# Kernel optimization log

Hardware: AMD Instinct MI355X
Metric: run time of the kernel (lower is better)

## Reference

```python
import jax, jax.numpy as jnp
import numpy as np

B, T, E = 4, 2_000_000, 8
C, K, STRIDE = 128, 512, 512
CHUNK, OVERLAP = 64000, 511  # overlap defaults to kernel_size - 1


def _candidate_positions(T):
    """Exact set of window start positions visited by the chunked streaming max.

    Replays the chunk loop of _lowmem_max_over_time: chunk starts advance by
    step = chunk_size - overlap (not a multiple of stride!), and within each
    chunk conv windows start at chunk_start + stride*k.
    """
    step = max(1, CHUNK - OVERLAP)
    pos = []
    start = 0
    while start < T:
        end = min(start + CHUNK, T)
        end_ext = min(end + OVERLAP, T)
        L = end_ext - start
        if L >= K:
            n = (L - K) // STRIDE + 1
            pos.append(start + STRIDE * np.arange(n, dtype=np.int64))
        if end == T:
            break
        start += step
    p = np.unique(np.concatenate(pos))
    return np.clip(p, 0, max(0, T - K))


POS = _candidate_positions(T)                       # [P] static window starts
WIN_IDX = POS[:, None] + np.arange(K, dtype=np.int64)  # [P, K] gather indices


def setup_inputs() -> dict:
    key = jax.random.key(0)
    ks = jax.random.split(key, 5)
    scale = 1.0 / float(np.sqrt(E * K))  # torch Conv1d default init range
    return {
        "x": jax.random.normal(ks[0], (B, T, E), dtype=jnp.float32),
        "w1": jax.random.uniform(ks[1], (C, E, K), jnp.float32, -scale, scale),
        "b1": jax.random.uniform(ks[2], (C,), jnp.float32, -scale, scale),
        "w2": jax.random.uniform(ks[3], (C, E, K), jnp.float32, -scale, scale),
        "b2": jax.random.uniform(ks[4], (C,), jnp.float32, -scale, scale),
    }


def reference(x, w1, b1, w2, b2):
    # Gather every candidate window the chunked scan would see: [B, P, K, E]
    wins = x[:, WIN_IDX, :]
    # Original clones windows under no_grad (stop_grad_input=True): input gets no grad.
    wins = jax.lax.stop_gradient(wins)
    # Gated conv (GLU): conv1(z) * sigmoid(conv2(z)) at each window -> [B, C, P]
    c1 = jnp.einsum('bpke,cek->bcp', wins, w1) + b1[:, None]
    c2 = jnp.einsum('bpke,cek->bcp', wins, w2) + b2[:, None]
    g = c1 * jax.nn.sigmoid(c2)
    # Global max-over-time per (batch, channel); identical value to the
    # running-max pass followed by exact re-evaluation at argmax positions.
    return g.max(axis=-1)  # [B, C]
```

## Files before the change

### kernel.cpp

```cpp
#include <hip/hip_runtime.h>


#define T_LEN 2000000
#define P_CNT 3937
#define M_TOT 15748
#define KD    4096

typedef __attribute__((ext_vector_type(8))) short short8;
typedef __attribute__((ext_vector_type(4))) float f32x4;

static __device__ __forceinline__ unsigned short f2bf(float f) {
    unsigned u = __builtin_bit_cast(unsigned, f);
    unsigned r = (u + 0x7FFFu + ((u >> 16) & 1u)) >> 16;
    return (unsigned short)r;
}

static __device__ __forceinline__ unsigned ordenc(float f) {
    unsigned u = __builtin_bit_cast(unsigned, f);
    return (u & 0x80000000u) ? ~u : (u | 0x80000000u);
}

static __device__ __forceinline__ size_t row_base(int m) {
    if (m > M_TOT - 1) m = M_TOT - 1;
    int bb = m / P_CNT;
    int p  = m - bb * P_CNT;
    int j, kp;
    if (p < 3875) { j = p / 125; kp = p - j * 125; }
    else          { j = 31;      kp = p - 3875; }
    long pos = (long)j * 63489 + (long)kp * 512;
    return ((size_t)bb * T_LEN + (size_t)pos) * 8u;
}

#define GLD_LDS16(gp, lp)                                                      \
    __builtin_amdgcn_global_load_lds(                                          \
        (const __attribute__((address_space(1))) void*)(gp),                   \
        (__attribute__((address_space(3))) void*)(lp), 16, 0, 0)

__global__ __launch_bounds__(256) void pack_w(const float* __restrict__ w1,
                                              const float* __restrict__ w2,
                                              unsigned short* __restrict__ Bp,
                                              unsigned* __restrict__ outu) {
    int idx = blockIdx.x * 256 + threadIdx.x;
    if (idx < 512) outu[idx] = 0u;
    if (idx >= 256 * KD) return;
    int n = idx >> 12;
    int k = idx & 4095;
    int e = k & 7;
    int t = k >> 3;
    const float* src = (n < 128) ? w1 : w2;
    Bp[idx] = f2bf(src[(n & 127) * 4096 + e * 512 + t]);
}

__global__ __launch_bounds__(512, 4) void gemm_max(const float* __restrict__ x,
                                                   const unsigned short* __restrict__ Bp,
                                                   const float* __restrict__ b1,
                                                   const float* __restrict__ b2,
                                                   unsigned* __restrict__ outu) {
    __shared__ __align__(16) char smem[73728];

    const int t  = threadIdx.x;
    const int m0 = blockIdx.x * 32;

    const int w    = t >> 6;
    const int lane = t & 63;
    const int wm   = w >> 2;
    const int wn   = w & 3;

    const int rA  = t >> 4;
    const int kcA = t & 15;
    const size_t aoff  = row_base(m0 + rA) + (size_t)(kcA * 4);
    const int    awoff = (rA * 128 + kcA * 8) ^ ((rA & 7) << 4);

    const unsigned short* bsrc[4];
    int bdst[4];
#pragma unroll
    for (int i = 0; i < 4; ++i) {
        int d  = i * 8192 + w * 1024 + lane * 16;
        int n  = d >> 7;
        int kc = ((d >> 4) & 7) ^ (n & 7);
        bsrc[i] = Bp + n * KD + kc * 8;
        bdst[i] = i * 8192 + w * 1024;
    }

    f32x4 acc[4];
#pragma unroll
    for (int nf = 0; nf < 4; ++nf) acc[nf] = (f32x4){0.f, 0.f, 0.f, 0.f};

    {
        float4 a0 = *(const float4*)(x + aoff);
#pragma unroll
        for (int i = 0; i < 4; ++i) GLD_LDS16(bsrc[i], smem + 8192 + bdst[i]);
        ushort4 h;
        h.x = f2bf(a0.x); h.y = f2bf(a0.y); h.z = f2bf(a0.z); h.w = f2bf(a0.w);
        *(ushort4*)(smem + awoff) = h;
    }
    __syncthreads();

    for (int ks = 0; ks < 64; ++ks) {
        const int cur = ks & 1;
        const int As  = cur * 4096;
        const int Bs  = 8192 + cur * 32768;
        float4 an;
        if (ks < 63) {
            const int kk = (ks + 1) * 64;
            an = *(const float4*)(x + aoff + kk);
            const int Bsn = 8192 + (cur ^ 1) * 32768;
#pragma unroll
            for (int i = 0; i < 4; ++i) GLD_LDS16(bsrc[i] + kk, smem + Bsn + bdst[i]);
        }
#pragma unroll
        for (int kq = 0; kq < 2; ++kq) {
            short8 af, bfr[4];
            {
                int r    = wm * 16 + (lane & 15);
                int boff = (r * 128 + kq * 64 + (lane >> 4) * 16) ^ ((r & 7) << 4);
                af = *(const short8*)(smem + As + boff);
            }
#pragma unroll
            for (int nf = 0; nf < 4; ++nf) {
                int n    = wn * 64 + nf * 16 + (lane & 15);
                int boff = (n * 128 + kq * 64 + (lane >> 4) * 16) ^ ((n & 7) << 4);
                bfr[nf] = *(const short8*)(smem + Bs + boff);
            }
#pragma unroll
            for (int nf = 0; nf < 4; ++nf)
                acc[nf] = __builtin_amdgcn_mfma_f32_16x16x32_bf16(
                    af, bfr[nf], acc[nf], 0, 0, 0);
        }
        if (ks < 63) {
            const int Asn = (cur ^ 1) * 4096;
            ushort4 h;
            h.x = f2bf(an.x); h.y = f2bf(an.y); h.z = f2bf(an.z); h.w = f2bf(an.w);
            *(ushort4*)(smem + Asn + awoff) = h;
        }
        __syncthreads();
    }

    float* gt = (float*)smem;
#pragma unroll
    for (int nf = 0; nf < 4; ++nf) {
        int col = wn * 64 + nf * 16 + (lane & 15);
#pragma unroll
        for (int q = 0; q < 4; ++q) {
            int row = wm * 16 + (lane >> 4) * 4 + q;
            gt[row * 256 + col] = acc[nf][q];
        }
    }
    __syncthreads();

    if (t < 128) {
        const int   c   = t;
        const float bb1 = b1[c];
        const float bb2 = b2[c];
        int   bprev = (m0 < M_TOT ? m0 : M_TOT - 1) / P_CNT;
        float best  = -3.4e38f;
        for (int r = 0; r < 32; ++r) {
            int m = m0 + r;
            if (m > M_TOT - 1) m = M_TOT - 1;
            int bb = m / P_CNT;
            float c1 = gt[r * 256 + c] + bb1;
            float c2 = gt[r * 256 + 128 + c] + bb2;
            float g  = c1 / (1.f + __expf(-c2));
            if (bb != bprev) {
                atomicMax(&outu[bprev * 128 + c], ordenc(best));
                bprev = bb;
                best  = -3.4e38f;
            }
            best = fmaxf(best, g);
        }
        atomicMax(&outu[bprev * 128 + c], ordenc(best));
    }
}

__global__ __launch_bounds__(256) void unmap_out(unsigned* __restrict__ outu) {
    int i = blockIdx.x * 256 + threadIdx.x;
    if (i < 512) {
        unsigned u = outu[i];
        outu[i] = (u & 0x80000000u) ? (u ^ 0x80000000u) : ~u;
    }
}

extern "C" void kernel_launch(void* const* d_in, const int* in_sizes, int n_in,
                              void* d_out, int out_size, void* d_ws, size_t ws_size,
                              hipStream_t stream) {
    const float* x  = (const float*)d_in[0];
    const float* w1 = (const float*)d_in[1];
    const float* b1 = (const float*)d_in[2];
    const float* w2 = (const float*)d_in[3];
    const float* b2 = (const float*)d_in[4];

    unsigned short* Bp   = (unsigned short*)d_ws;
    unsigned*       outu = (unsigned*)d_out;

    pack_w<<<dim3((256 * KD) / 256), dim3(256), 0, stream>>>(w1, w2, Bp, outu);

    const int nblk = (M_TOT + 31) / 32;
    gemm_max<<<dim3(nblk), dim3(512), 0, stream>>>(x, Bp, b1, b2, outu);

    unmap_out<<<dim3(2), dim3(256), 0, stream>>>(outu);
}
```

Before: 84.61 us.

## Load fp32 A tile directly to LDS via global_load_lds with manual vmcnt waits

```diff
diff --git a/kernel.cpp b/kernel.cpp
--- a/kernel.cpp
+++ b/kernel.cpp
@@ -35,6 +35,12 @@
     __builtin_amdgcn_global_load_lds(                                          \
         (const __attribute__((address_space(1))) void*)(gp),                   \
         (__attribute__((address_space(3))) void*)(lp), 16, 0, 0)
+
+#define FENCE()   asm volatile("" ::: "memory")
+#define WAITVM5() asm volatile("s_waitcnt vmcnt(5)" ::: "memory")
+#define WAITVM0() asm volatile("s_waitcnt vmcnt(0)" ::: "memory")
+#define WAITLGKM0() asm volatile("s_waitcnt lgkmcnt(0)" ::: "memory")
+#define BARRIER() do { FENCE(); __builtin_amdgcn_s_barrier(); FENCE(); } while (0)
 
 __global__ __launch_bounds__(256) void pack_w(const float* __restrict__ w1,
                                               const float* __restrict__ w2,
@@ -56,7 +62,7 @@
                                                    const float* __restrict__ b1,
                                                    const float* __restrict__ b2,
                                                    unsigned* __restrict__ outu) {
-    __shared__ __align__(16) char smem[73728];
+    __shared__ __align__(16) char smem[81920];
 
     const int t  = threadIdx.x;
     const int m0 = blockIdx.x * 32;
@@ -66,10 +72,9 @@
     const int wm   = w >> 2;
     const int wn   = w & 3;
 
-    const int rA  = t >> 4;
-    const int kcA = t & 15;
-    const size_t aoff  = row_base(m0 + rA) + (size_t)(kcA * 4);
-    const int    awoff = (rA * 128 + kcA * 8) ^ ((rA & 7) << 4);
+    const int    rowA  = t >> 4;
+    const size_t asrc0 = row_base(m0 + rowA) + (size_t)((((t & 15) ^ (rowA & 7)) * 4));
+    const int    adst  = w * 1024;
 
     const unsigned short* bsrc[4];
     int bdst[4];
@@ -86,55 +91,67 @@
 #pragma unroll
     for (int nf = 0; nf < 4; ++nf) acc[nf] = (f32x4){0.f, 0.f, 0.f, 0.f};
 
-    {
-        float4 a0 = *(const float4*)(x + aoff);
-#pragma unroll
-        for (int i = 0; i < 4; ++i) GLD_LDS16(bsrc[i], smem + 8192 + bdst[i]);
-        ushort4 h;
-        h.x = f2bf(a0.x); h.y = f2bf(a0.y); h.z = f2bf(a0.z); h.w = f2bf(a0.w);
-        *(ushort4*)(smem + awoff) = h;
-    }
-    __syncthreads();
+    const int rA    = wm * 16 + (lane & 15);
+    const int qA    = lane >> 4;
+    int aro[2];
+#pragma unroll
+    for (int kq = 0; kq < 2; ++kq)
+        aro[kq] = (rA * 256 + kq * 128 + qA * 32) ^ ((rA & 7) << 4);
+    int bro[2][4];
+#pragma unroll
+    for (int kq = 0; kq < 2; ++kq)
+#pragma unroll
+        for (int nf = 0; nf < 4; ++nf) {
+            int n = wn * 64 + nf * 16 + (lane & 15);
+            bro[kq][nf] = (n * 128 + kq * 64 + (lane >> 4) * 16) ^ ((n & 7) << 4);
+        }
+
+#pragma unroll
+    for (int i = 0; i < 4; ++i) GLD_LDS16(bsrc[i], smem + 16384 + bdst[i]);
+    GLD_LDS16(x + asrc0, smem + adst);
+    FENCE();
 
     for (int ks = 0; ks < 64; ++ks) {
         const int cur = ks & 1;
-        const int As  = cur * 4096;
-        const int Bs  = 8192 + cur * 32768;
-        float4 an;
+        const int As  = cur * 8192;
+        const int Bs  = 16384 + cur * 32768;
         if (ks < 63) {
-            const int kk = (ks + 1) * 64;
-            an = *(const float4*)(x + aoff + kk);
-            const int Bsn = 8192 + (cur ^ 1) * 32768;
+            const int kk  = (ks + 1) * 64;
+            const int Asn = (cur ^ 1) * 8192;
+            const int Bsn = 16384 + (cur ^ 1) * 32768;
 #pragma unroll
             for (int i = 0; i < 4; ++i) GLD_LDS16(bsrc[i] + kk, smem + Bsn + bdst[i]);
-        }
+            GLD_LDS16(x + asrc0 + kk, smem + Asn + adst);
+            FENCE();
+            WAITVM5();
+        } else {
+            WAITVM0();
+        }
+        BARRIER();
+
 #pragma unroll
         for (int kq = 0; kq < 2; ++kq) {
-            short8 af, bfr[4];
-            {
-                int r    = wm * 16 + (lane & 15);
-                int boff = (r * 128 + kq * 64 + (lane >> 4) * 16) ^ ((r & 7) << 4);
-                af = *(const short8*)(smem + As + boff);
-            }
-#pragma unroll
-            for (int nf = 0; nf < 4; ++nf) {
-                int n    = wn * 64 + nf * 16 + (lane & 15);
-                int boff = (n * 128 + kq * 64 + (lane >> 4) * 16) ^ ((n & 7) << 4);
-                bfr[nf] = *(const short8*)(smem + Bs + boff);
-            }
+            float4 f0 = *(const float4*)(smem + As + aro[kq]);
+            float4 f1 = *(const float4*)(smem + As + (aro[kq] ^ 16));
+            short8 af;
+            af[0] = (short)f2bf(f0.x); af[1] = (short)f2bf(f0.y);
+            af[2] = (short)f2bf(f0.z); af[3] = (short)f2bf(f0.w);
+            af[4] = (short)f2bf(f1.x); af[5] = (short)f2bf(f1.y);
+            af[6] = (short)f2bf(f1.z); af[7] = (short)f2bf(f1.w);
+            short8 bfr[4];
+#pragma unroll
+            for (int nf = 0; nf < 4; ++nf)
+                bfr[nf] = *(const short8*)(smem + Bs + bro[kq][nf]);
 #pragma unroll
             for (int nf = 0; nf < 4; ++nf)
                 acc[nf] = __builtin_amdgcn_mfma_f32_16x16x32_bf16(
                     af, bfr[nf], acc[nf], 0, 0, 0);
         }
-        if (ks < 63) {
-            const int Asn = (cur ^ 1) * 4096;
-            ushort4 h;
-            h.x = f2bf(an.x); h.y = f2bf(an.y); h.z = f2bf(an.z); h.w = f2bf(an.w);
-            *(ushort4*)(smem + Asn + awoff) = h;
-        }
-        __syncthreads();
-    }
+        WAITLGKM0();
+        BARRIER();
+    }
+
+    __syncthreads();
 
     float* gt = (float*)smem;
 #pragma unroll
```

Result: slower. 93.98 us (+11.1%).

## Prefetch A tile two stages ahead with manual waitcnt barriers

Applied to the files above, without the earlier changes.

```diff
diff --git a/kernel.cpp b/kernel.cpp
--- a/kernel.cpp
+++ b/kernel.cpp
@@ -35,6 +35,11 @@
     __builtin_amdgcn_global_load_lds(                                          \
         (const __attribute__((address_space(1))) void*)(gp),                   \
         (__attribute__((address_space(3))) void*)(lp), 16, 0, 0)
+
+#define FENCE()     asm volatile("" ::: "memory")
+#define WAITVM1()   asm volatile("s_waitcnt vmcnt(1)" ::: "memory")
+#define WAITVM0()   asm volatile("s_waitcnt vmcnt(0)" ::: "memory")
+#define WAITLGKM0() asm volatile("s_waitcnt lgkmcnt(0)" ::: "memory")
 
 __global__ __launch_bounds__(256) void pack_w(const float* __restrict__ w1,
                                               const float* __restrict__ w2,
@@ -66,10 +71,10 @@
     const int wm   = w >> 2;
     const int wn   = w & 3;
 
-    const int rA  = t >> 4;
+    const int rAs = t >> 4;
     const int kcA = t & 15;
-    const size_t aoff  = row_base(m0 + rA) + (size_t)(kcA * 4);
-    const int    awoff = (rA * 128 + kcA * 8) ^ ((rA & 7) << 4);
+    const size_t aoff  = row_base(m0 + rAs) + (size_t)(kcA * 4);
+    const int    awoff = (rAs * 128 + kcA * 8) ^ ((rAs & 7) << 4);
 
     const unsigned short* bsrc[4];
     int bdst[4];
@@ -86,54 +91,80 @@
 #pragma unroll
     for (int nf = 0; nf < 4; ++nf) acc[nf] = (f32x4){0.f, 0.f, 0.f, 0.f};
 
+    const int rA = wm * 16 + (lane & 15);
+    int aro[2];
+#pragma unroll
+    for (int kq = 0; kq < 2; ++kq)
+        aro[kq] = (rA * 128 + kq * 64 + (lane >> 4) * 16) ^ ((rA & 7) << 4);
+    int bro[2][4];
+#pragma unroll
+    for (int kq = 0; kq < 2; ++kq)
+#pragma unroll
+        for (int nf = 0; nf < 4; ++nf) {
+            int n = wn * 64 + nf * 16 + (lane & 15);
+            bro[kq][nf] = (n * 128 + kq * 64 + (lane >> 4) * 16) ^ ((n & 7) << 4);
+        }
+
+#pragma unroll
+    for (int i = 0; i < 4; ++i) GLD_LDS16(bsrc[i], smem + 8192 + bdst[i]);
+    FENCE();
+    float4 a0 = *(const float4*)(x + aoff);
+    FENCE();
+    float4 anext = *(const float4*)(x + aoff + 64);
+    FENCE();
     {
-        float4 a0 = *(const float4*)(x + aoff);
-#pragma unroll
-        for (int i = 0; i < 4; ++i) GLD_LDS16(bsrc[i], smem + 8192 + bdst[i]);
         ushort4 h;
         h.x = f2bf(a0.x); h.y = f2bf(a0.y); h.z = f2bf(a0.z); h.w = f2bf(a0.w);
         *(ushort4*)(smem + awoff) = h;
     }
-    __syncthreads();
+    WAITLGKM0();
+    FENCE();
+    __builtin_amdgcn_s_barrier();
+    FENCE();
 
     for (int ks = 0; ks < 64; ++ks) {
         const int cur = ks & 1;
         const int As  = cur * 4096;
         const int Bs  = 8192 + cur * 32768;
-        float4 an;
+        const int Asn = (cur ^ 1) * 4096;
+        const int Bsn = 8192 + (cur ^ 1) * 32768;
+
         if (ks < 63) {
             const int kk = (ks + 1) * 64;
-            an = *(const float4*)(x + aoff + kk);
-            const int Bsn = 8192 + (cur ^ 1) * 32768;
 #pragma unroll
             for (int i = 0; i < 4; ++i) GLD_LDS16(bsrc[i] + kk, smem + Bsn + bdst[i]);
         }
+        FENCE();
+        float4 anext2 = anext;
+        if (ks < 62) anext2 = *(const float4*)(x + aoff + (size_t)(ks + 2) * 64);
+        FENCE();
+
 #pragma unroll
         for (int kq = 0; kq < 2; ++kq) {
-            short8 af, bfr[4];
-            {
-                int r    = wm * 16 + (lane & 15);
-                int boff = (r * 128 + kq * 64 + (lane >> 4) * 16) ^ ((r & 7) << 4);
-                af = *(const short8*)(smem + As + boff);
-            }
-#pragma unroll
-            for (int nf = 0; nf < 4; ++nf) {
-                int n    = wn * 64 + nf * 16 + (lane & 15);
-                int boff = (n * 128 + kq * 64 + (lane >> 4) * 16) ^ ((n & 7) << 4);
-                bfr[nf] = *(const short8*)(smem + Bs + boff);
-            }
+            short8 af = *(const short8*)(smem + As + aro[kq]);
+            short8 bfr[4];
+#pragma unroll
+            for (int nf = 0; nf < 4; ++nf)
+                bfr[nf] = *(const short8*)(smem + Bs + bro[kq][nf]);
 #pragma unroll
             for (int nf = 0; nf < 4; ++nf)
                 acc[nf] = __builtin_amdgcn_mfma_f32_16x16x32_bf16(
                     af, bfr[nf], acc[nf], 0, 0, 0);
         }
+
         if (ks < 63) {
-            const int Asn = (cur ^ 1) * 4096;
             ushort4 h;
-            h.x = f2bf(an.x); h.y = f2bf(an.y); h.z = f2bf(an.z); h.w = f2bf(an.w);
+            h.x = f2bf(anext.x); h.y = f2bf(anext.y);
+            h.z = f2bf(anext.z); h.w = f2bf(anext.w);
             *(ushort4*)(smem + Asn + awoff) = h;
         }
-        __syncthreads();
+        anext = anext2;
+
+        if (ks < 62) { WAITVM1(); } else { WAITVM0(); }
+        WAITLGKM0();
+        FENCE();
+        __builtin_amdgcn_s_barrier();
+        FENCE();
     }
 
     float* gt = (float*)smem;
```

Result: no change. 85.57 us (+1.1%).

## Drop LDS staging; load MFMA fragments directly from global with register double-buffering

Applied to the files above, without the earlier changes.

```diff
diff --git a/kernel.cpp b/kernel.cpp
--- a/kernel.cpp
+++ b/kernel.cpp
@@ -31,121 +31,132 @@
     return ((size_t)bb * T_LEN + (size_t)pos) * 8u;
 }
 
-#define GLD_LDS16(gp, lp)                                                      \
-    __builtin_amdgcn_global_load_lds(                                          \
-        (const __attribute__((address_space(1))) void*)(gp),                   \
-        (__attribute__((address_space(3))) void*)(lp), 16, 0, 0)
+static __device__ __forceinline__ short8 cvt8(float4 lo, float4 hi) {
+    unsigned d0, d1, d2, d3;
+    asm("v_cvt_pk_bf16_f32 %0, %1, %2" : "=v"(d0) : "v"(lo.x), "v"(lo.y));
+    asm("v_cvt_pk_bf16_f32 %0, %1, %2" : "=v"(d1) : "v"(lo.z), "v"(lo.w));
+    asm("v_cvt_pk_bf16_f32 %0, %1, %2" : "=v"(d2) : "v"(hi.x), "v"(hi.y));
+    asm("v_cvt_pk_bf16_f32 %0, %1, %2" : "=v"(d3) : "v"(hi.z), "v"(hi.w));
+    uint4 u; u.x = d0; u.y = d1; u.z = d2; u.w = d3;
+    return __builtin_bit_cast(short8, u);
+}
 
 __global__ __launch_bounds__(256) void pack_w(const float* __restrict__ w1,
                                               const float* __restrict__ w2,
-                                              unsigned short* __restrict__ Bp,
+                                              uint4* __restrict__ Bpf,
                                               unsigned* __restrict__ outu) {
-    int idx = blockIdx.x * 256 + threadIdx.x;
-    if (idx < 512) outu[idx] = 0u;
-    if (idx >= 256 * KD) return;
-    int n = idx >> 12;
-    int k = idx & 4095;
-    int e = k & 7;
-    int t = k >> 3;
+    int c = blockIdx.x * 256 + threadIdx.x;
+    if (c < 512) outu[c] = 0u;
+    if (c >= 131072) return;
+    int l  = c & 63;
+    int nt = (c >> 6) & 15;
+    int kq = (c >> 10) & 1;
+    int ks = c >> 11;
+    int n  = nt * 16 + (l & 15);
+    int kb = ks * 64 + kq * 32 + ((l >> 4) << 3);
     const float* src = (n < 128) ? w1 : w2;
-    Bp[idx] = f2bf(src[(n & 127) * 4096 + e * 512 + t]);
-}
-
-__global__ __launch_bounds__(512, 4) void gemm_max(const float* __restrict__ x,
-                                                   const unsigned short* __restrict__ Bp,
+    int cc = n & 127;
+    unsigned short h[8];
+#pragma unroll
+    for (int j = 0; j < 8; ++j) {
+        int k = kb + j;
+        h[j] = f2bf(src[cc * 4096 + (k & 7) * 512 + (k >> 3)]);
+    }
+    uint4 v;
+    v.x = (unsigned)h[0] | ((unsigned)h[1] << 16);
+    v.y = (unsigned)h[2] | ((unsigned)h[3] << 16);
+    v.z = (unsigned)h[4] | ((unsigned)h[5] << 16);
+    v.w = (unsigned)h[6] | ((unsigned)h[7] << 16);
+    Bpf[c] = v;
+}
+
+#define LOAD_A(FA, ks)                                                         \
+    do {                                                                       \
+        _Pragma("unroll")                                                      \
+        for (int mf = 0; mf < 2; ++mf) {                                       \
+            const char* ab = xb + (mf ? a1 : a0) + (size_t)((ks) * 256);       \
+            _Pragma("unroll")                                                  \
+            for (int kq = 0; kq < 2; ++kq) {                                   \
+                FA[mf][kq][0] = *(const float4*)(ab + kq * 128);               \
+                FA[mf][kq][1] = *(const float4*)(ab + kq * 128 + 16);          \
+            }                                                                  \
+        }                                                                      \
+    } while (0)
+
+#define LOAD_B(BB, ks)                                                         \
+    do {                                                                       \
+        _Pragma("unroll")                                                      \
+        for (int kq = 0; kq < 2; ++kq)                                         \
+            _Pragma("unroll")                                                  \
+            for (int nf = 0; nf < 4; ++nf)                                     \
+                BB[kq][nf] = Bq[((ks) * 2 + kq) * 1024 + bbase + nf * 64];     \
+    } while (0)
+
+#define COMPUTE(FA, BB)                                                        \
+    do {                                                                       \
+        _Pragma("unroll")                                                      \
+        for (int kq = 0; kq < 2; ++kq) {                                       \
+            short8 af0 = cvt8(FA[0][kq][0], FA[0][kq][1]);                     \
+            short8 af1 = cvt8(FA[1][kq][0], FA[1][kq][1]);                     \
+            _Pragma("unroll")                                                  \
+            for (int nf = 0; nf < 4; ++nf) {                                   \
+                short8 bf = __builtin_bit_cast(short8, BB[kq][nf]);            \
+                acc[0][nf] = __builtin_amdgcn_mfma_f32_16x16x32_bf16(          \
+                    af0, bf, acc[0][nf], 0, 0, 0);                             \
+                acc[1][nf] = __builtin_amdgcn_mfma_f32_16x16x32_bf16(          \
+                    af1, bf, acc[1][nf], 0, 0, 0);                             \
+            }                                                                  \
+        }                                                                      \
+    } while (0)
+
+__global__ __launch_bounds__(256, 2) void gemm_max(const float* __restrict__ x,
+                                                   const uint4* __restrict__ Bq,
                                                    const float* __restrict__ b1,
                                                    const float* __restrict__ b2,
                                                    unsigned* __restrict__ outu) {
-    __shared__ __align__(16) char smem[73728];
-
-    const int t  = threadIdx.x;
-    const int m0 = blockIdx.x * 32;
-
-    const int w    = t >> 6;
+    __shared__ float gt[32 * 256];
+
+    const int t    = threadIdx.x;
     const int lane = t & 63;
-    const int wm   = w >> 2;
-    const int wn   = w & 3;
-
-    const int rA  = t >> 4;
-    const int kcA = t & 15;
-    const size_t aoff  = row_base(m0 + rA) + (size_t)(kcA * 4);
-    const int    awoff = (rA * 128 + kcA * 8) ^ ((rA & 7) << 4);
-
-    const unsigned short* bsrc[4];
-    int bdst[4];
-#pragma unroll
-    for (int i = 0; i < 4; ++i) {
-        int d  = i * 8192 + w * 1024 + lane * 16;
-        int n  = d >> 7;
-        int kc = ((d >> 4) & 7) ^ (n & 7);
-        bsrc[i] = Bp + n * KD + kc * 8;
-        bdst[i] = i * 8192 + w * 1024;
-    }
-
-    f32x4 acc[4];
-#pragma unroll
-    for (int nf = 0; nf < 4; ++nf) acc[nf] = (f32x4){0.f, 0.f, 0.f, 0.f};
-
-    {
-        float4 a0 = *(const float4*)(x + aoff);
-#pragma unroll
-        for (int i = 0; i < 4; ++i) GLD_LDS16(bsrc[i], smem + 8192 + bdst[i]);
-        ushort4 h;
-        h.x = f2bf(a0.x); h.y = f2bf(a0.y); h.z = f2bf(a0.z); h.w = f2bf(a0.w);
-        *(ushort4*)(smem + awoff) = h;
-    }
-    __syncthreads();
-
-    for (int ks = 0; ks < 64; ++ks) {
-        const int cur = ks & 1;
-        const int As  = cur * 4096;
-        const int Bs  = 8192 + cur * 32768;
-        float4 an;
-        if (ks < 63) {
-            const int kk = (ks + 1) * 64;
-            an = *(const float4*)(x + aoff + kk);
-            const int Bsn = 8192 + (cur ^ 1) * 32768;
-#pragma unroll
-            for (int i = 0; i < 4; ++i) GLD_LDS16(bsrc[i] + kk, smem + Bsn + bdst[i]);
+    const int wn   = t >> 6;
+    const int m0   = blockIdx.x * 32;
+
+    const char*  xb = (const char*)x;
+    const size_t a0 = row_base(m0 + (lane & 15)) * 4 + (size_t)((lane >> 4) * 32);
+    const size_t a1 = row_base(m0 + 16 + (lane & 15)) * 4 + (size_t)((lane >> 4) * 32);
+    const int bbase = wn * 4 * 64 + lane;
+
+    f32x4 acc[2][4];
+#pragma unroll
+    for (int mf = 0; mf < 2; ++mf)
+#pragma unroll
+        for (int nf = 0; nf < 4; ++nf) acc[mf][nf] = (f32x4){0.f, 0.f, 0.f, 0.f};
+
+    float4 fAX[2][2][2], fAY[2][2][2];
+    uint4  bBX[2][4],    bBY[2][4];
+
+    LOAD_A(fAX, 0);
+    LOAD_B(bBX, 0);
+
+#pragma unroll 2
+    for (int ks = 0; ks < 64; ks += 2) {
+        if (ks + 1 < 64) { LOAD_A(fAY, ks + 1); LOAD_B(bBY, ks + 1); }
+        COMPUTE(fAX, bBX);
+        if (ks + 2 < 64) { LOAD_A(fAX, ks + 2); LOAD_B(bBX, ks + 2); }
+        COMPUTE(fAY, bBY);
+    }
+
+#pragma unroll
+    for (int mf = 0; mf < 2; ++mf)
+#pragma unroll
+        for (int nf = 0; nf < 4; ++nf) {
+            int col = wn * 64 + nf * 16 + (lane & 15);
+#pragma unroll
+            for (int q = 0; q < 4; ++q) {
+                int row = mf * 16 + (lane >> 4) * 4 + q;
+                gt[row * 256 + col] = acc[mf][nf][q];
+            }
         }
-#pragma unroll
-        for (int kq = 0; kq < 2; ++kq) {
-            short8 af, bfr[4];
-            {
-                int r    = wm * 16 + (lane & 15);
-                int boff = (r * 128 + kq * 64 + (lane >> 4) * 16) ^ ((r & 7) << 4);
-                af = *(const short8*)(smem + As + boff);
-            }
-#pragma unroll
-            for (int nf = 0; nf < 4; ++nf) {
-                int n    = wn * 64 + nf * 16 + (lane & 15);
-                int boff = (n * 128 + kq * 64 + (lane >> 4) * 16) ^ ((n & 7) << 4);
-                bfr[nf] = *(const short8*)(smem + Bs + boff);
-            }
-#pragma unroll
-            for (int nf = 0; nf < 4; ++nf)
-                acc[nf] = __builtin_amdgcn_mfma_f32_16x16x32_bf16(
-                    af, bfr[nf], acc[nf], 0, 0, 0);
-        }
-        if (ks < 63) {
-            const int Asn = (cur ^ 1) * 4096;
-            ushort4 h;
-            h.x = f2bf(an.x); h.y = f2bf(an.y); h.z = f2bf(an.z); h.w = f2bf(an.w);
-            *(ushort4*)(smem + Asn + awoff) = h;
-        }
-        __syncthreads();
-    }
-
-    float* gt = (float*)smem;
-#pragma unroll
-    for (int nf = 0; nf < 4; ++nf) {
-        int col = wn * 64 + nf * 16 + (lane & 15);
-#pragma unroll
-        for (int q = 0; q < 4; ++q) {
-            int row = wm * 16 + (lane >> 4) * 4 + q;
-            gt[row * 256 + col] = acc[nf][q];
-        }
-    }
     __syncthreads();
 
     if (t < 128) {
@@ -189,13 +200,13 @@
     const float* w2 = (const float*)d_in[3];
     const float* b2 = (const float*)d_in[4];
 
-    unsigned short* Bp   = (unsigned short*)d_ws;
-    unsigned*       outu = (unsigned*)d_out;
-
-    pack_w<<<dim3((256 * KD) / 256), dim3(256), 0, stream>>>(w1, w2, Bp, outu);
+    uint4*    Bpf  = (uint4*)d_ws;
+    unsigned* outu = (unsigned*)d_out;
+
+    pack_w<<<dim3(512), dim3(256), 0, stream>>>(w1, w2, Bpf, outu);
 
     const int nblk = (M_TOT + 31) / 32;
-    gemm_max<<<dim3(nblk), dim3(512), 0, stream>>>(x, Bp, b1, b2, outu);
+    gemm_max<<<dim3(nblk), dim3(256), 0, stream>>>(x, (const uint4*)Bpf, b1, b2, outu);
 
     unmap_out<<<dim3(2), dim3(256), 0, stream>>>(outu);
 }
```

New measurement: 171.9 us. +103.2%, slower.
